# Optimization experiments

Hardware: AMD Instinct MI355X
Metric: run time of the kernel (lower is better)

Reference implementation:

```python
import jax, jax.numpy as jnp
import numpy as np

B, N, C = 4, 2048, 1024
H = 16
HD = C // H
SCALE = HD ** -0.5


def setup_inputs() -> dict:
    key = jax.random.key(0)
    ks = jax.random.split(key, 5)
    s = 0.02
    return {
        "x": jax.random.normal(ks[0], (B, N, C), dtype=jnp.float32),
        "w_qkv": jax.random.normal(ks[1], (C, 3 * C), dtype=jnp.float32) * s,
        "b_qkv": jnp.zeros((3 * C,), dtype=jnp.float32),
        "w_proj": jax.random.normal(ks[2], (C, C), dtype=jnp.float32) * s,
        "b_proj": jnp.zeros((C,), dtype=jnp.float32),
    }


def reference(x, w_qkv, b_qkv, w_proj, b_proj):
    b, n, c = x.shape
    qkv = x @ w_qkv + b_qkv                       # [b, n, 3c]
    qkv = qkv.reshape(b, n, 3, H, HD)
    qkv = jnp.transpose(qkv, (2, 0, 3, 1, 4))     # [3, b, h, n, hd]
    q, k, v = qkv[0], qkv[1], qkv[2]
    attn = jnp.einsum("bhqd,bhkd->bhqk", q, k) * SCALE
    attn = jax.nn.softmax(attn, axis=-1)
    out = jnp.einsum("bhqk,bhkd->bhqd", attn, v)  # [b, h, n, hd]
    out = jnp.transpose(out, (0, 2, 1, 3)).reshape(b, n, c)
    return out @ w_proj + b_proj
```

## Files before the change

### kernel.cpp

```cpp
#include <hip/hip_runtime.h>
#include <cstdint>
#include <cstddef>


typedef __attribute__((ext_vector_type(8))) short short8;
typedef __attribute__((ext_vector_type(4))) float f32x4;
typedef _Float16 half4 __attribute__((ext_vector_type(4)));

#if __has_builtin(__builtin_amdgcn_exp2f)
#define EXP2F(x) __builtin_amdgcn_exp2f(x)
#else
#define EXP2F(x) __expf((x) * 0.69314718056f)
#endif

__device__ __forceinline__ short f2bf(float x) {
  unsigned u = __builtin_bit_cast(unsigned, x);
  u += 0x7fffu + ((u >> 16) & 1u);
  return (short)(u >> 16);
}

__device__ __forceinline__ unsigned pkh(float a, float b) {
  auto h = __builtin_amdgcn_cvt_pkrtz(a, b);
  return __builtin_bit_cast(unsigned, h);
}

__device__ __forceinline__ void async16(const void* g, void* l) {
  __builtin_amdgcn_global_load_lds(
      (const __attribute__((address_space(1))) unsigned*)g,
      (__attribute__((address_space(3))) unsigned*)l, 16, 0, 0);
}


__global__ __launch_bounds__(256) void convert_kernel(const float* __restrict__ in,
                                                      short* __restrict__ out) {
  int i = blockIdx.x * 256 + threadIdx.x;
  const float4* p = (const float4*)in + (size_t)i * 2;
  float4 a = p[0], b = p[1];
  short8 r;
  r[0] = f2bf(a.x); r[1] = f2bf(a.y); r[2] = f2bf(a.z); r[3] = f2bf(a.w);
  r[4] = f2bf(b.x); r[5] = f2bf(b.y); r[6] = f2bf(b.z); r[7] = f2bf(b.w);
  *((short8*)out + i) = r;
}

__global__ __launch_bounds__(256) void wtrans_kernel(const float* __restrict__ in,
                                                     short* __restrict__ out,
                                                     int K, int N) {
  __shared__ float tile[32][33];
  int n0 = blockIdx.x * 32, k0 = blockIdx.y * 32;
  int tx = threadIdx.x, ty = threadIdx.y;
  for (int r = ty; r < 32; r += 8)
    tile[r][tx] = in[(size_t)(k0 + r) * N + n0 + tx];
  __syncthreads();
  for (int r = ty; r < 32; r += 8)
    out[(size_t)(n0 + r) * K + k0 + tx] = f2bf(tile[tx][r]);
}


template <int MODE>
__global__ __launch_bounds__(512, 2) void gemm_kernel(
    const short* __restrict__ A, const short* __restrict__ Bt,
    const float* __restrict__ bias, int Nn,
    short* __restrict__ qb, short* __restrict__ kb, short* __restrict__ vtb,
    float* __restrict__ outp) {
  constexpr int K = 1024;
  constexpr int NT = K / 64;
  __shared__ __align__(16) short As[3][256 * 64];
  __shared__ __align__(16) short Bs[3][128 * 64];
  const int tid = threadIdx.x, wave = tid >> 6, lane = tid & 63;
  const int quad = lane >> 4, l16 = lane & 15;
  const int m0 = blockIdx.y * 256, n0 = blockIdx.x * 128;
  const int wrow = (wave >> 1) * 64, wcol = (wave & 1) * 64;

  const int srow = tid >> 3;
  const int schunk = ((tid & 7) ^ (srow & 7)) * 8;
  const short* Ag = A + (size_t)(m0 + srow) * K + schunk;
  const short* Bg = Bt + (size_t)(n0 + srow) * K + schunk;
  const int fsw = l16 & 7;

  f32x4 acc[4][4] = {};
  short8 af[4][2], bf[2][2];

  auto stageA = [&](int b, int kt) {
#pragma unroll
    for (int i = 0; i < 4; ++i)
      async16(Ag + (size_t)(i * 64) * K + kt * 64,
              (char*)As[b] + i * 8192 + tid * 16);
  };
  auto stageB = [&](int b, int kt) {
#pragma unroll
    for (int i = 0; i < 2; ++i)
      async16(Bg + (size_t)(i * 64) * K + kt * 64,
              (char*)Bs[b] + i * 8192 + tid * 16);
  };

  stageA(0, 0); stageB(0, 0);
  stageA(1, 1); stageB(1, 1);
  asm volatile("s_waitcnt vmcnt(6)" ::: "memory");
  __builtin_amdgcn_s_barrier();

  int cb = 0;
  for (int t = 0; t < NT; ++t) {
    int sb = cb + 2; if (sb >= 3) sb -= 3;
    const short* Ab = As[cb];
    const short* Bb = Bs[cb];

#pragma unroll
    for (int mf = 0; mf < 4; ++mf)
#pragma unroll
      for (int ks = 0; ks < 2; ++ks)
        af[mf][ks] = *(const short8*)
            &Ab[(wrow + mf * 16 + l16) * 64 + (((ks * 4 + quad) ^ fsw) << 3)];
#pragma unroll
    for (int j = 0; j < 2; ++j)
#pragma unroll
      for (int ks = 0; ks < 2; ++ks)
        bf[j][ks] = *(const short8*)
            &Bb[(wcol + j * 16 + l16) * 64 + (((ks * 4 + quad) ^ fsw) << 3)];
    if (t + 2 < NT) stageA(sb, t + 2);
    __builtin_amdgcn_s_barrier();
    __builtin_amdgcn_s_setprio(1);
#pragma unroll
    for (int ks = 0; ks < 2; ++ks)
#pragma unroll
      for (int mf = 0; mf < 4; ++mf)
#pragma unroll
        for (int j = 0; j < 2; ++j)
          acc[mf][j] = __builtin_amdgcn_mfma_f32_16x16x32_bf16(
              af[mf][ks], bf[j][ks], acc[mf][j], 0, 0, 0);
    __builtin_amdgcn_s_setprio(0);
    __builtin_amdgcn_s_barrier();

#pragma unroll
    for (int j = 0; j < 2; ++j)
#pragma unroll
      for (int ks = 0; ks < 2; ++ks)
        bf[j][ks] = *(const short8*)
            &Bb[(wcol + (2 + j) * 16 + l16) * 64 + (((ks * 4 + quad) ^ fsw) << 3)];
    if (t + 2 < NT) stageB(sb, t + 2);
    __builtin_amdgcn_s_barrier();
    __builtin_amdgcn_s_setprio(1);
#pragma unroll
    for (int ks = 0; ks < 2; ++ks)
#pragma unroll
      for (int mf = 0; mf < 4; ++mf)
#pragma unroll
        for (int j = 0; j < 2; ++j)
          acc[mf][2 + j] = __builtin_amdgcn_mfma_f32_16x16x32_bf16(
              af[mf][ks], bf[j][ks], acc[mf][2 + j], 0, 0, 0);
    __builtin_amdgcn_s_setprio(0);
    if (t < NT - 2)
      asm volatile("s_waitcnt vmcnt(6)" ::: "memory");
    else if (t == NT - 2)
      asm volatile("s_waitcnt vmcnt(0)" ::: "memory");
    __builtin_amdgcn_s_barrier();
    cb = cb + 1; if (cb >= 3) cb -= 3;
  }

  if (MODE == 0) {
#pragma unroll
    for (int mf = 0; mf < 4; ++mf) {
      int row0 = m0 + wrow + mf * 16 + quad * 4;
      int b = row0 >> 11, n = row0 & 2047;
#pragma unroll
      for (int nf = 0; nf < 4; ++nf) {
        int col = n0 + wcol + nf * 16 + l16;
        float bv = bias[col];
        float v0 = acc[mf][nf][0] + bv, v1 = acc[mf][nf][1] + bv;
        float v2 = acc[mf][nf][2] + bv, v3 = acc[mf][nf][3] + bv;
        int which = col >> 10;
        int h = (col >> 6) & 15;
        int d = col & 63;
        size_t bh = (size_t)(b * 16 + h);
        if (which == 0) {
          const float qs = 0.18033688f;
          size_t base = (bh * 2048 + n) * 64 + d;
          qb[base]       = f2bf(v0 * qs);
          qb[base + 64]  = f2bf(v1 * qs);
          qb[base + 128] = f2bf(v2 * qs);
          qb[base + 192] = f2bf(v3 * qs);
        } else if (which == 1) {
          size_t base = (bh * 2048 + n) * 64 + d;
          kb[base]       = f2bf(v0);
          kb[base + 64]  = f2bf(v1);
          kb[base + 128] = f2bf(v2);
          kb[base + 192] = f2bf(v3);
        } else {
          uint2 pk;
          pk.x = pkh(v0, v1);
          pk.y = pkh(v2, v3);
          *(uint2*)&vtb[(bh * 64 + d) * 2048 + n] = pk;
        }
      }
    }
  } else {
#pragma unroll
    for (int mf = 0; mf < 4; ++mf) {
      int row0 = m0 + wrow + mf * 16 + quad * 4;
#pragma unroll
      for (int nf = 0; nf < 4; ++nf) {
        int col = n0 + wcol + nf * 16 + l16;
        float bv = bias[col];
        outp[(size_t)row0 * Nn + col]       = acc[mf][nf][0] + bv;
        outp[(size_t)(row0 + 1) * Nn + col] = acc[mf][nf][1] + bv;
        outp[(size_t)(row0 + 2) * Nn + col] = acc[mf][nf][2] + bv;
        outp[(size_t)(row0 + 3) * Nn + col] = acc[mf][nf][3] + bv;
      }
    }
  }
}


__global__ __launch_bounds__(256, 4) void attn_kernel(
    const short* __restrict__ qb, const short* __restrict__ kb,
    const short* __restrict__ vtb, short* __restrict__ ob) {
  __shared__ __align__(16) short Ks[2][64 * 64];
  __shared__ __align__(16) short Vs[2][64 * 64];
  __shared__ __align__(16) float Ls[4][32];
  const int tid = threadIdx.x, wave = tid >> 6, lane = tid & 63;
  const int quad = lane >> 4, l16 = lane & 15;
  const int q0 = blockIdx.x * 128;
  const int bh = blockIdx.y;
  const short* Qg = qb + (size_t)bh * (2048 * 64);
  const short* Kg = kb + (size_t)bh * (2048 * 64);
  const short* Vg = vtb + (size_t)bh * (64 * 2048);

  short8 qf[2][2];
#pragma unroll
  for (int qt = 0; qt < 2; ++qt)
#pragma unroll
    for (int kc = 0; kc < 2; ++kc)
      qf[qt][kc] = *(const short8*)
          &Qg[(size_t)(q0 + wave * 32 + qt * 16 + l16) * 64 + kc * 32 + quad * 8];

  const int str = lane >> 3;
  const int sgc = ((lane & 7) ^ (str & 7)) * 8;
  const int fsw = l16 & 7;
  const int c0 = wave * 2, c1 = wave * 2 + 1;

  async16(Kg + (size_t)(c0 * 8 + str) * 64 + sgc, (char*)Ks[0] + c0 * 1024);
  async16(Kg + (size_t)(c1 * 8 + str) * 64 + sgc, (char*)Ks[0] + c1 * 1024);
  async16(Vg + (size_t)(c0 * 8 + str) * 2048 + sgc, (char*)Vs[0] + c0 * 1024);
  async16(Vg + (size_t)(c1 * 8 + str) * 2048 + sgc, (char*)Vs[0] + c1 * 1024);

  float lsum[2] = {0.f, 0.f};
  f32x4 oacc[2][4] = {};

  for (int t = 0; t < 32; ++t) {
    __syncthreads();

    int kvn = (t + 1) * 64;
    if (kvn < 2048) {
      char* kd = (char*)Ks[(t + 1) & 1];
      char* vd = (char*)Vs[(t + 1) & 1];
      async16(Kg + (size_t)(kvn + c0 * 8 + str) * 64 + sgc, kd + c0 * 1024);
      async16(Kg + (size_t)(kvn + c1 * 8 + str) * 64 + sgc, kd + c1 * 1024);
      async16(Vg + (size_t)(c0 * 8 + str) * 2048 + kvn + sgc, vd + c0 * 1024);
      async16(Vg + (size_t)(c1 * 8 + str) * 2048 + kvn + sgc, vd + c1 * 1024);
    }
    const short* Kst = Ks[t & 1];
    const short* Vst = Vs[t & 1];

    f32x4 sacc[2][4] = {};
#pragma unroll
    for (int kc = 0; kc < 2; ++kc) {
      short8 kf[4];
#pragma unroll
      for (int kvt = 0; kvt < 4; ++kvt)
        kf[kvt] = *(const short8*)
            &Kst[(kvt * 16 + l16) * 64 + (((kc * 4 + quad) ^ fsw) << 3)];
#pragma unroll
      for (int kvt = 0; kvt < 4; ++kvt)
#pragma unroll
        for (int qt = 0; qt < 2; ++qt)
          sacc[qt][kvt] = __builtin_amdgcn_mfma_f32_16x16x32_bf16(
              kf[kvt], qf[qt][kc], sacc[qt][kvt], 0, 0, 0);
    }

#pragma unroll
    for (int kvt = 0; kvt < 4; ++kvt) {
      half4 pfr[2];
#pragma unroll
      for (int qt = 0; qt < 2; ++qt) {
        float p0 = EXP2F(sacc[qt][kvt][0]);
        float p1 = EXP2F(sacc[qt][kvt][1]);
        float p2 = EXP2F(sacc[qt][kvt][2]);
        float p3 = EXP2F(sacc[qt][kvt][3]);
        lsum[qt] += (p0 + p1) + (p2 + p3);
        uint2 w;
        w.x = pkh(p0, p1);
        w.y = pkh(p2, p3);
        pfr[qt] = __builtin_bit_cast(half4, w);
      }
      const int vcol = (((kvt * 2 + (quad >> 1)) ^ fsw) << 3) + (quad & 1) * 4;
#pragma unroll
      for (int nt = 0; nt < 4; ++nt) {
        uint2 vr = *(const uint2*)&Vst[(nt * 16 + l16) * 64 + vcol];
        half4 vfr = __builtin_bit_cast(half4, vr);
#pragma unroll
        for (int qt = 0; qt < 2; ++qt)
          oacc[qt][nt] = __builtin_amdgcn_mfma_f32_16x16x16f16(
              pfr[qt], vfr, oacc[qt][nt], 0, 0, 0);
      }
    }
  }

#pragma unroll
  for (int qt = 0; qt < 2; ++qt) {
    float v = lsum[qt];
    v += __shfl_xor(v, 16, 64);
    v += __shfl_xor(v, 32, 64);
    if (quad == 0) Ls[wave][qt * 16 + l16] = v;
  }
  __asm__ volatile("s_waitcnt lgkmcnt(0)" ::: "memory");
  __builtin_amdgcn_wave_barrier();

  const int b = bh >> 4, h = bh & 15;
#pragma unroll
  for (int qt = 0; qt < 2; ++qt) {
    float4 lr = *(const float4*)&Ls[wave][qt * 16 + quad * 4];
    float inv0 = 1.f / lr.x, inv1 = 1.f / lr.y, inv2 = 1.f / lr.z, inv3 = 1.f / lr.w;
#pragma unroll
    for (int nt = 0; nt < 4; ++nt) {
      int d = nt * 16 + l16;
      int qbase = q0 + wave * 32 + qt * 16 + quad * 4;
      size_t obase = ((size_t)(b * 2048 + qbase)) * 1024 + h * 64 + d;
      ob[obase]        = f2bf(oacc[qt][nt][0] * inv0);
      ob[obase + 1024] = f2bf(oacc[qt][nt][1] * inv1);
      ob[obase + 2048] = f2bf(oacc[qt][nt][2] * inv2);
      ob[obase + 3072] = f2bf(oacc[qt][nt][3] * inv3);
    }
  }
}


extern "C" void kernel_launch(void* const* d_in, const int* in_sizes, int n_in,
                              void* d_out, int out_size, void* d_ws, size_t ws_size,
                              hipStream_t stream) {
  const float* x      = (const float*)d_in[0];
  const float* w_qkv  = (const float*)d_in[1];
  const float* b_qkv  = (const float*)d_in[2];
  const float* w_proj = (const float*)d_in[3];
  const float* b_proj = (const float*)d_in[4];
  float* out = (float*)d_out;

  short* xs     = (short*)d_ws;
  short* wqkvT  = xs + (size_t)8192 * 1024;
  short* wprojT = wqkvT + (size_t)3072 * 1024;
  short* qb     = wprojT + (size_t)1024 * 1024;
  short* kb     = qb + (size_t)64 * 2048 * 64;
  short* vtb    = kb + (size_t)64 * 2048 * 64;
  short* aob    = vtb + (size_t)64 * 2048 * 64;

  convert_kernel<<<dim3(4096), 256, 0, stream>>>(x, xs);
  wtrans_kernel<<<dim3(96, 32), dim3(32, 8), 0, stream>>>(w_qkv, wqkvT, 1024, 3072);
  wtrans_kernel<<<dim3(32, 32), dim3(32, 8), 0, stream>>>(w_proj, wprojT, 1024, 1024);

  gemm_kernel<0><<<dim3(24, 32), 512, 0, stream>>>(xs, wqkvT, b_qkv, 3072,
                                                   qb, kb, vtb, nullptr);
  attn_kernel<<<dim3(16, 64), 256, 0, stream>>>(qb, kb, vtb, aob);
  gemm_kernel<1><<<dim3(8, 32), 512, 0, stream>>>(aob, wprojT, b_proj, 1024,
                                                  nullptr, nullptr, nullptr, out);
}
```

Before: 288.4 us.

## Use 8 waves per attention block with one query tile each, remap blocks for XCD locality

The attention kernel moves from 4 waves each handling 32 query rows to 8 waves each handling 16 rows, so each block keeps 128 rows but every thread issues one async K/V load per tile instead of two. Block indices are also permuted so consecutive blocks on the same XCD share a batch-head, meant to improve L2 reuse of K/V. Per-wave work and register use shrink, which allows more waves in flight. In exchange each K fragment read from LDS is reused for one query tile instead of two, so LDS traffic per MFMA doubles.

```diff
diff --git a/kernel.cpp b/kernel.cpp
--- a/kernel.cpp
+++ b/kernel.cpp
@@ -210,57 +210,52 @@
 }
 
 
-__global__ __launch_bounds__(256, 4) void attn_kernel(
+__global__ __launch_bounds__(512, 8) void attn_kernel(
     const short* __restrict__ qb, const short* __restrict__ kb,
     const short* __restrict__ vtb, short* __restrict__ ob) {
   __shared__ __align__(16) short Ks[2][64 * 64];
   __shared__ __align__(16) short Vs[2][64 * 64];
-  __shared__ __align__(16) float Ls[4][32];
+  __shared__ __align__(16) float Ls[8][16];
   const int tid = threadIdx.x, wave = tid >> 6, lane = tid & 63;
   const int quad = lane >> 4, l16 = lane & 15;
-  const int q0 = blockIdx.x * 128;
-  const int bh = blockIdx.y;
+  int n = blockIdx.x + blockIdx.y * 16;
+  n = (n & 7) * 128 + (n >> 3);
+  const int q0 = (n & 15) * 128;
+  const int bh = n >> 4;
   const short* Qg = qb + (size_t)bh * (2048 * 64);
   const short* Kg = kb + (size_t)bh * (2048 * 64);
   const short* Vg = vtb + (size_t)bh * (64 * 2048);
 
-  short8 qf[2][2];
-#pragma unroll
-  for (int qt = 0; qt < 2; ++qt)
-#pragma unroll
-    for (int kc = 0; kc < 2; ++kc)
-      qf[qt][kc] = *(const short8*)
-          &Qg[(size_t)(q0 + wave * 32 + qt * 16 + l16) * 64 + kc * 32 + quad * 8];
-
-  const int str = lane >> 3;
-  const int sgc = ((lane & 7) ^ (str & 7)) * 8;
+  short8 qf[2];
+#pragma unroll
+  for (int kc = 0; kc < 2; ++kc)
+    qf[kc] = *(const short8*)
+        &Qg[(size_t)(q0 + wave * 16 + l16) * 64 + kc * 32 + quad * 8];
+
+  const int srow = tid >> 3;
+  const int sgc = ((tid & 7) ^ (srow & 7)) * 8;
   const int fsw = l16 & 7;
-  const int c0 = wave * 2, c1 = wave * 2 + 1;
-
-  async16(Kg + (size_t)(c0 * 8 + str) * 64 + sgc, (char*)Ks[0] + c0 * 1024);
-  async16(Kg + (size_t)(c1 * 8 + str) * 64 + sgc, (char*)Ks[0] + c1 * 1024);
-  async16(Vg + (size_t)(c0 * 8 + str) * 2048 + sgc, (char*)Vs[0] + c0 * 1024);
-  async16(Vg + (size_t)(c1 * 8 + str) * 2048 + sgc, (char*)Vs[0] + c1 * 1024);
-
-  float lsum[2] = {0.f, 0.f};
-  f32x4 oacc[2][4] = {};
+
+  async16(Kg + (size_t)srow * 64 + sgc, (char*)Ks[0] + tid * 16);
+  async16(Vg + (size_t)srow * 2048 + sgc, (char*)Vs[0] + tid * 16);
+
+  float lsum = 0.f;
+  f32x4 oacc[4] = {};
 
   for (int t = 0; t < 32; ++t) {
     __syncthreads();
 
     int kvn = (t + 1) * 64;
     if (kvn < 2048) {
-      char* kd = (char*)Ks[(t + 1) & 1];
-      char* vd = (char*)Vs[(t + 1) & 1];
-      async16(Kg + (size_t)(kvn + c0 * 8 + str) * 64 + sgc, kd + c0 * 1024);
-      async16(Kg + (size_t)(kvn + c1 * 8 + str) * 64 + sgc, kd + c1 * 1024);
-      async16(Vg + (size_t)(c0 * 8 + str) * 2048 + kvn + sgc, vd + c0 * 1024);
-      async16(Vg + (size_t)(c1 * 8 + str) * 2048 + kvn + sgc, vd + c1 * 1024);
+      async16(Kg + (size_t)(kvn + srow) * 64 + sgc,
+              (char*)Ks[(t + 1) & 1] + tid * 16);
+      async16(Vg + (size_t)srow * 2048 + kvn + sgc,
+              (char*)Vs[(t + 1) & 1] + tid * 16);
     }
     const short* Kst = Ks[t & 1];
     const short* Vst = Vs[t & 1];
 
-    f32x4 sacc[2][4] = {};
+    f32x4 sacc[4] = {};
 #pragma unroll
     for (int kc = 0; kc < 2; ++kc) {
       short8 kf[4];
@@ -270,64 +265,54 @@
             &Kst[(kvt * 16 + l16) * 64 + (((kc * 4 + quad) ^ fsw) << 3)];
 #pragma unroll
       for (int kvt = 0; kvt < 4; ++kvt)
-#pragma unroll
-        for (int qt = 0; qt < 2; ++qt)
-          sacc[qt][kvt] = __builtin_amdgcn_mfma_f32_16x16x32_bf16(
-              kf[kvt], qf[qt][kc], sacc[qt][kvt], 0, 0, 0);
+        sacc[kvt] = __builtin_amdgcn_mfma_f32_16x16x32_bf16(
+            kf[kvt], qf[kc], sacc[kvt], 0, 0, 0);
     }
 
 #pragma unroll
     for (int kvt = 0; kvt < 4; ++kvt) {
-      half4 pfr[2];
-#pragma unroll
-      for (int qt = 0; qt < 2; ++qt) {
-        float p0 = EXP2F(sacc[qt][kvt][0]);
-        float p1 = EXP2F(sacc[qt][kvt][1]);
-        float p2 = EXP2F(sacc[qt][kvt][2]);
-        float p3 = EXP2F(sacc[qt][kvt][3]);
-        lsum[qt] += (p0 + p1) + (p2 + p3);
-        uint2 w;
-        w.x = pkh(p0, p1);
-        w.y = pkh(p2, p3);
-        pfr[qt] = __builtin_bit_cast(half4, w);
-      }
+      float p0 = EXP2F(sacc[kvt][0]);
+      float p1 = EXP2F(sacc[kvt][1]);
+      float p2 = EXP2F(sacc[kvt][2]);
+      float p3 = EXP2F(sacc[kvt][3]);
+      lsum += (p0 + p1) + (p2 + p3);
+      uint2 w;
+      w.x = pkh(p0, p1);
+      w.y = pkh(p2, p3);
+      half4 pfr = __builtin_bit_cast(half4, w);
       const int vcol = (((kvt * 2 + (quad >> 1)) ^ fsw) << 3) + (quad & 1) * 4;
 #pragma unroll
       for (int nt = 0; nt < 4; ++nt) {
         uint2 vr = *(const uint2*)&Vst[(nt * 16 + l16) * 64 + vcol];
         half4 vfr = __builtin_bit_cast(half4, vr);
-#pragma unroll
-        for (int qt = 0; qt < 2; ++qt)
-          oacc[qt][nt] = __builtin_amdgcn_mfma_f32_16x16x16f16(
-              pfr[qt], vfr, oacc[qt][nt], 0, 0, 0);
+        oacc[nt] = __builtin_amdgcn_mfma_f32_16x16x16f16(
+            pfr, vfr, oacc[nt], 0, 0, 0);
       }
     }
   }
 
-#pragma unroll
-  for (int qt = 0; qt < 2; ++qt) {
-    float v = lsum[qt];
+  {
+    float v = lsum;
     v += __shfl_xor(v, 16, 64);
     v += __shfl_xor(v, 32, 64);
-    if (quad == 0) Ls[wave][qt * 16 + l16] = v;
+    if (quad == 0) Ls[wave][l16] = v;
   }
   __asm__ volatile("s_waitcnt lgkmcnt(0)" ::: "memory");
   __builtin_amdgcn_wave_barrier();
 
   const int b = bh >> 4, h = bh & 15;
-#pragma unroll
-  for (int qt = 0; qt < 2; ++qt) {
-    float4 lr = *(const float4*)&Ls[wave][qt * 16 + quad * 4];
+  {
+    float4 lr = *(const float4*)&Ls[wave][quad * 4];
     float inv0 = 1.f / lr.x, inv1 = 1.f / lr.y, inv2 = 1.f / lr.z, inv3 = 1.f / lr.w;
 #pragma unroll
     for (int nt = 0; nt < 4; ++nt) {
       int d = nt * 16 + l16;
-      int qbase = q0 + wave * 32 + qt * 16 + quad * 4;
+      int qbase = q0 + wave * 16 + quad * 4;
       size_t obase = ((size_t)(b * 2048 + qbase)) * 1024 + h * 64 + d;
-      ob[obase]        = f2bf(oacc[qt][nt][0] * inv0);
-      ob[obase + 1024] = f2bf(oacc[qt][nt][1] * inv1);
-      ob[obase + 2048] = f2bf(oacc[qt][nt][2] * inv2);
-      ob[obase + 3072] = f2bf(oacc[qt][nt][3] * inv3);
+      ob[obase]        = f2bf(oacc[nt][0] * inv0);
+      ob[obase + 1024] = f2bf(oacc[nt][1] * inv1);
+      ob[obase + 2048] = f2bf(oacc[nt][2] * inv2);
+      ob[obase + 3072] = f2bf(oacc[nt][3] * inv3);
     }
   }
 }
@@ -357,7 +342,7 @@
 
   gemm_kernel<0><<<dim3(24, 32), 512, 0, stream>>>(xs, wqkvT, b_qkv, 3072,
                                                    qb, kb, vtb, nullptr);
-  attn_kernel<<<dim3(16, 64), 256, 0, stream>>>(qb, kb, vtb, aob);
+  attn_kernel<<<dim3(16, 64), 512, 0, stream>>>(qb, kb, vtb, aob);
   gemm_kernel<1><<<dim3(8, 32), 512, 0, stream>>>(aob, wprojT, b_proj, 1024,
                                                   nullptr, nullptr, nullptr, out);
 }
```

Measured after the change: 294.9 us. 1.02x slower.
